# Optimization experiments

Hardware: AMD Instinct MI355X
Metric: run time of the kernel (lower is better)

The kernel has to match this reference:

```python
import jax, jax.numpy as jnp
import numpy as np

B, NQ, T = 1, 16, 512
L, D, H, HD, FF = 8, 512, 8, 64, 2048
LAT, CB, CBD = 1024, 2048, 256


def _rms(x, w, eps=1e-6):
    xf = x.astype(jnp.float32)
    y = xf * jax.lax.rsqrt(jnp.mean(xf * xf, axis=-1, keepdims=True) + eps)
    return y.astype(x.dtype) * w


def _rot_half(x):
    x1, x2 = jnp.split(x, 2, axis=-1)
    return jnp.concatenate((-x2, x1), axis=-1)


def _conv(x, w, b, pad):
    # x: [B, W, Cin], w: [K, Cin, Cout]
    return jax.lax.conv_general_dilated(x, w, (1,), pad, dimension_numbers=('NWC', 'WIO', 'NWC')) + b


def _convT(x, w, b, s):
    # output length = input length * s (SAME-padded transposed conv)
    return jax.lax.conv_transpose(x, w, (s,), 'SAME', dimension_numbers=('NWC', 'WIO', 'NWC')) + b


def setup_inputs() -> dict:
    key = jax.random.key(0)
    ks = iter(jax.random.split(key, 64))
    p = lambda *s: 0.02 * jax.random.normal(next(ks), s, jnp.float32)
    return dict(
        codes=jax.random.randint(next(ks), (B, NQ, T), 0, CB),
        emb_first=p(CB, CBD), pf_w=p(CBD, LAT), pf_b=p(LAT),
        fo_w=p(LAT, LAT), fo_b=p(LAT),
        emb_rest=p(NQ - 1, CB, CBD), pr_w=p(NQ - 1, CBD, LAT), pr_b=p(NQ - 1, LAT),
        ro_w=p(LAT, LAT), ro_b=p(LAT),
        pre_w=p(3, LAT, LAT), pre_b=p(LAT),
        in_w=p(LAT, D), in_b=p(D),
        ln1=jnp.ones((L, D)), qw=p(L, D, D), kw=p(L, D, D), vw=p(L, D, D), ow=p(L, D, D),
        qn=jnp.ones((L, HD)), kn=jnp.ones((L, HD)),
        ls_a=jnp.full((L, D), 0.1), ln2=jnp.ones((L, D)),
        w1=p(L, D, FF), w2=p(L, FF, D), ls_m=jnp.full((L, D), 0.1),
        fn_w=jnp.ones((D,)), out_w=p(D, LAT), out_b=p(LAT),
        up_w=p(4, LAT, LAT), up_b=p(LAT),
        dec0_w=p(7, LAT, 512), dec0_b=p(512),
        dw1=p(16, 512, 256), db1=p(256),
        dw2=p(12, 256, 128), db2=p(128),
        dw3=p(10, 128, 64), db3=p(64),
        dw4=p(8, 64, 32), db4=p(32),
        fin_w=p(7, 32, 1), fin_b=p(1),
    )


def reference(codes, emb_first, pf_w, pf_b, fo_w, fo_b, emb_rest, pr_w, pr_b, ro_w, ro_b,
              pre_w, pre_b, in_w, in_b, ln1, qw, kw, vw, ow, qn, kn, ls_a, ln2, w1, w2,
              ls_m, fn_w, out_w, out_b, up_w, up_b, dec0_w, dec0_b,
              dw1, db1, dw2, db2, dw3, db3, dw4, db4, fin_w, fin_b):
    Bc, _, Tc = codes.shape
    # --- RVQ decode (unrolled codebook lookups + 1x1 output projections) ---
    qf = jnp.take(emb_first, codes[:, 0], axis=0)            # [B,T,CBD]
    qf = qf @ pf_w + pf_b                                    # project_out -> [B,T,LAT]
    qf = qf @ fo_w + fo_b                                    # first_output_proj
    codes_rest = jnp.swapaxes(codes[:, 1:], 0, 1)            # [NQ-1,B,T]
    g = jax.vmap(lambda e, c: jnp.take(e, c, axis=0))(emb_rest, codes_rest)  # [NQ-1,B,T,CBD]
    qr = jnp.einsum('nbtc,ncd->btd', g, pr_w) + jnp.sum(pr_b, axis=0)
    qr = qr @ ro_w + ro_b                                    # rest_output_proj
    hidden = qf + qr                                         # [B,T,LAT]
    # --- causal pre_conv (k=3, left pad) ---
    hidden = _conv(hidden, pre_w, pre_b, [(2, 0)])
    # --- pre_transformer: RoPE + qk-norm + layerscale, manual causal attention ---
    h = hidden @ in_w + in_b                                 # [B,T,D]
    pos = jnp.arange(Tc, dtype=jnp.float32)
    inv_freq = 1.0 / (10000.0 ** (jnp.arange(0, HD, 2, dtype=jnp.float32) / HD))
    freqs = pos[:, None] * inv_freq[None, :]                 # [T,HD/2]
    emb = jnp.concatenate((freqs, freqs), axis=-1)           # [T,HD]
    cos, sin = jnp.cos(emb), jnp.sin(emb)
    mask = jnp.triu(jnp.full((Tc, Tc), -jnp.inf, dtype=jnp.float32), k=1)
    scale = HD ** -0.5
    for l in range(L):
        x = _rms(h, ln1[l])
        q = _rms((x @ qw[l]).reshape(Bc, Tc, H, HD), qn[l]).transpose(0, 2, 1, 3)
        k = _rms((x @ kw[l]).reshape(Bc, Tc, H, HD), kn[l]).transpose(0, 2, 1, 3)
        v = (x @ vw[l]).reshape(Bc, Tc, H, HD).transpose(0, 2, 1, 3)
        q = q * cos + _rot_half(q) * sin
        k = k * cos + _rot_half(k) * sin
        scores = jnp.einsum('bhqd,bhkd->bhqk', q, k) * scale + mask
        a = jax.nn.softmax(scores.astype(jnp.float32), axis=-1).astype(x.dtype)
        o = jnp.einsum('bhqk,bhkd->bhqd', a, v).transpose(0, 2, 1, 3).reshape(Bc, Tc, D)
        h = h + ls_a[l] * (o @ ow[l])
        x = _rms(h, ln2[l])
        h = h + ls_m[l] * (jax.nn.gelu(x @ w1[l], approximate=False) @ w2[l])
    h = _rms(h, fn_w) @ out_w + out_b                        # [B,T,LAT]
    # --- upsample x2 ---
    x = jax.nn.elu(_convT(h, up_w, up_b, 2))
    x = _conv(x, dec0_w, dec0_b, 'SAME')
    for w, b, r in ((dw1, db1, 8), (dw2, db2, 6), (dw3, db3, 5), (dw4, db4, 4)):
        x = _convT(jax.nn.elu(x), w, b, r)
    x = _conv(jax.nn.elu(x), fin_w, fin_b, 'SAME')           # [B,S,1]
    return jnp.clip(jnp.swapaxes(x, 1, 2), -1.0, 1.0)        # [B,1,S]
```

## Files before the change

### kernel.cpp

```cpp
#include <hip/hip_runtime.h>
#include <hip/hip_bf16.h>
#include <math.h>

#define T_LEN 512
#define LAT   1024
#define D_DIM 512
#define NH    8
#define HD    64
#define FF_D  2048
#define NL    8
#define NQ    16

typedef _Float16 f16x4 __attribute__((ext_vector_type(4)));
typedef _Float16 f16x8 __attribute__((ext_vector_type(8)));
typedef float    f32x4 __attribute__((ext_vector_type(4)));

#define WS_QFPRE    0
#define WS_G        131072
#define WS_QF       2097152
#define WS_TA       2621440
#define WS_HIDG     3145728
#define WS_HID      3147776
#define WS_CONV     3672064
#define WS_H        4196352
#define WS_X        4458496
#define WS_QB       4720640
#define WS_KB       4982784
#define WS_VB       5244928
#define WS_ATT      5507072
#define WS_FF       5769216
#define WS_BSUM     6817792
#define WS_HOUT     6819840
#define WS_UP       7348224
#define WS_DEC0     8400384
#define WS_T1       8925440
#define WS_T2       11022976
#define WS_W2UP     17314560
#define WS_W2D1     23606016
#define WS_W2D2     26751744
#define WS_W2D3     27341568
#define WS_T3       31457344
#define WS_W2D4     47186048
#define WS_T4       0
#define WS_DEC0B16  11022976
#define WS_PART     31457344
#define WS_BTPR     35651712
#define WS_ROPE     39583872

__global__ void k_zero_guards(float* __restrict__ ws) {
    const int offs[13] = {3145728, 6818816, 7344128, 7345152, 8396800,
                          8399872, 8924672, 8925184, 11022592, 11022848,
                          17314432, 31457280, 47185984};
    const int lens[13] = {2048, 1024, 1024, 3072, 3072,
                          512, 512, 256, 256, 128,
                          128, 64, 64};
    int r = blockIdx.x;
    for (int i = threadIdx.x; i < lens[r]; i += 256) ws[offs[r] + i] = 0.f;
}

__global__ __launch_bounds__(256) void k_gather(const int* __restrict__ codes,
                                                const float* __restrict__ emb_first,
                                                const float* __restrict__ emb_rest,
                                                float* __restrict__ qf_pre,
                                                float* __restrict__ G) {
    int idx = blockIdx.x * 256 + threadIdx.x;
    int c = idx & 255;
    int r = (idx >> 8) & 15;
    int t = idx >> 12;
    if (t >= T_LEN) return;
    if (r == 0) {
        int code = codes[t];
        qf_pre[t * 256 + c] = emb_first[code * 256 + c];
    } else {
        int n = r - 1;
        int code = codes[(n + 1) * T_LEN + t];
        G[t * 3840 + n * 256 + c] = emb_rest[(n * 2048 + code) * 256 + c];
    }
}

__global__ void k_bias_sum(const float* __restrict__ pr_b, float* __restrict__ out) {
    int d = blockIdx.x * 256 + threadIdx.x;
    if (d >= LAT) return;
    float s = 0.f;
    for (int n = 0; n < NQ - 1; n++) s += pr_b[n * LAT + d];
    out[d] = s;
}

__global__ void k_rope_tab(float* __restrict__ tab) {
    int idx = blockIdx.x * 256 + threadIdx.x;
    int t = idx >> 5, dm = idx & 31;
    double inv = pow(10000.0, -(double)dm / 32.0);
    double ang = (double)t * inv;
    tab[idx] = (float)cos(ang);
    tab[16384 + idx] = (float)sin(ang);
}

__global__ __launch_bounds__(256) void k_wt16(const float* __restrict__ w,
                                              _Float16* __restrict__ bth,
                                              _Float16* __restrict__ btl,
                                              int Cin, int Cout, int s, int pad_a) {
    int K3 = 3 * Cin;
    int col = blockIdx.x * 64 + (threadIdx.x & 63);
    int rk0 = blockIdx.y * 128 + (threadIdx.x >> 6) * 32;
    if (rk0 >= K3) return;
    int p = col / Cout, co = col - p * Cout;
    int kk0 = (pad_a - p) % s;
    if (kk0 < 0) kk0 += s;
    int cp = (p + kk0 - pad_a) / s;
    size_t ob = (size_t)col * K3 + rk0;
    for (int rb = 0; rb < 32; rb += 4) {
        f16x4 h, l;
#pragma unroll
        for (int j2 = 0; j2 < 4; ++j2) {
            int rowk = rk0 + rb + j2;
            int j = rowk / Cin, ci = rowk - j * Cin;
            int d = j - 1;
            float v = 0.f;
            if (d == cp) v = w[((size_t)kk0 * Cin + ci) * Cout + co];
            else if (d == cp + 1) v = w[((size_t)(kk0 + s) * Cin + ci) * Cout + co];
            _Float16 hh = (_Float16)v;
            h[j2] = hh;
            l[j2] = (_Float16)(v - (float)hh);
        }
        *(f16x4*)(bth + ob + rb) = h;
        *(f16x4*)(btl + ob + rb) = l;
    }
}

__global__ __launch_bounds__(256) void k_bt16(const float* __restrict__ w,
                                              _Float16* __restrict__ bth,
                                              _Float16* __restrict__ btl,
                                              int K, int N) {
    int col = blockIdx.x * 64 + (threadIdx.x & 63);
    int rk0 = blockIdx.y * 128 + (threadIdx.x >> 6) * 32;
    size_t ob = (size_t)col * K + rk0;
    for (int rb = 0; rb < 32; rb += 4) {
        f16x4 h, l;
#pragma unroll
        for (int j2 = 0; j2 < 4; ++j2) {
            float v = w[(size_t)(rk0 + rb + j2) * N + col];
            _Float16 hh = (_Float16)v;
            h[j2] = hh;
            l[j2] = (_Float16)(v - (float)hh);
        }
        *(f16x4*)(bth + ob + rb) = h;
        *(f16x4*)(btl + ob + rb) = l;
    }
}

__device__ __forceinline__ float apply_act(float v, int act) {
    if (act == 1) return 0.5f * v * (1.0f + erff(v * 0.70710678118654752440f));
    if (act == 2) return v > 0.f ? v : expm1f(v);
    return v;
}

__global__ __launch_bounds__(256) void k_gemm16(const float* __restrict__ A, int lda,
                                                const _Float16* __restrict__ BTh,
                                                const _Float16* __restrict__ BTl, int ldb,
                                                const float* __restrict__ bias, unsigned bmask,
                                                float* __restrict__ C,
                                                float* __restrict__ part, long mn,
                                                int N, int klen, int act) {
    __shared__ _Float16 Ash[128 * 64];
    __shared__ _Float16 Asl[128 * 64];
    __shared__ _Float16 Bsh[64 * 64];
    __shared__ _Float16 Bsl[64 * 64];
    int tid = threadIdx.x;
    int m0 = blockIdx.x * 128, n0 = blockIdx.y * 64;
    int kz = blockIdx.z * klen;
    const float* Ab = A + kz;
    int lane = tid & 63, wv = tid >> 6;
    int wr = wv >> 1, wc = wv & 1;
    int fr = lane & 15, g = lane >> 4;

    f32x4 acc[4][2];
#pragma unroll
    for (int m = 0; m < 4; ++m)
#pragma unroll
        for (int n = 0; n < 2; ++n)
#pragma unroll
            for (int r = 0; r < 4; ++r) acc[m][n][r] = 0.f;

    int nk = klen >> 6;
    for (int t = 0; t < nk; ++t) {
        int k0 = t << 6;
#pragma unroll
        for (int i2 = 0; i2 < 8; ++i2) {
            int c = tid + 256 * i2;
            int row = c >> 4, kc = c & 15;
            float4 v = *(const float4*)(Ab + (size_t)(m0 + row) * lda + k0 + (kc << 2));
            f16x4 h, l;
            float vv[4] = {v.x, v.y, v.z, v.w};
#pragma unroll
            for (int j = 0; j < 4; ++j) {
                _Float16 hh = (_Float16)vv[j];
                h[j] = hh;
                l[j] = (_Float16)(vv[j] - (float)hh);
            }
            int off = row * 64 + (((kc >> 1) ^ (row & 7)) << 3) + ((kc & 1) << 2);
            *(f16x4*)(Ash + off) = h;
            *(f16x4*)(Asl + off) = l;
        }
#pragma unroll
        for (int i2 = 0; i2 < 2; ++i2) {
            int c = tid + 256 * i2;
            int col = c >> 3, s = c & 7;
            size_t goff = (size_t)(n0 + col) * ldb + kz + k0 + (s << 3);
            f16x8 hv = *(const f16x8*)(BTh + goff);
            f16x8 lv = *(const f16x8*)(BTl + goff);
            int off = col * 64 + ((s ^ (col & 7)) << 3);
            *(f16x8*)(Bsh + off) = hv;
            *(f16x8*)(Bsl + off) = lv;
        }
        __syncthreads();
#pragma unroll
        for (int kk = 0; kk < 2; ++kk) {
            f16x8 ah[4], al[4], bh[2], bl[2];
#pragma unroll
            for (int m = 0; m < 4; ++m) {
                int row = wr * 64 + m * 16 + fr;
                int off = row * 64 + ((((kk << 2) + g) ^ (row & 7)) << 3);
                ah[m] = *(const f16x8*)(Ash + off);
                al[m] = *(const f16x8*)(Asl + off);
            }
#pragma unroll
            for (int n = 0; n < 2; ++n) {
                int col = wc * 32 + n * 16 + fr;
                int off = col * 64 + ((((kk << 2) + g) ^ (col & 7)) << 3);
                bh[n] = *(const f16x8*)(Bsh + off);
                bl[n] = *(const f16x8*)(Bsl + off);
            }
#pragma unroll
            for (int m = 0; m < 4; ++m)
#pragma unroll
                for (int n = 0; n < 2; ++n) {
                    acc[m][n] = __builtin_amdgcn_mfma_f32_16x16x32_f16(ah[m], bh[n], acc[m][n], 0, 0, 0);
                    acc[m][n] = __builtin_amdgcn_mfma_f32_16x16x32_f16(ah[m], bl[n], acc[m][n], 0, 0, 0);
                    acc[m][n] = __builtin_amdgcn_mfma_f32_16x16x32_f16(al[m], bh[n], acc[m][n], 0, 0, 0);
                }
        }
        __syncthreads();
    }
    if (part) {
        float* op = part + (size_t)blockIdx.z * mn;
#pragma unroll
        for (int m = 0; m < 4; ++m) {
            int row = m0 + wr * 64 + m * 16 + (g << 2);
#pragma unroll
            for (int n = 0; n < 2; ++n) {
                int col = n0 + wc * 32 + n * 16 + fr;
#pragma unroll
                for (int r = 0; r < 4; ++r)
                    op[(size_t)(row + r) * N + col] = acc[m][n][r];
            }
        }
    } else {
#pragma unroll
        for (int m = 0; m < 4; ++m) {
            int row = m0 + wr * 64 + m * 16 + (g << 2);
#pragma unroll
            for (int n = 0; n < 2; ++n) {
                int col = n0 + wc * 32 + n * 16 + fr;
                float bv = bias ? bias[col & bmask] : 0.f;
#pragma unroll
                for (int r = 0; r < 4; ++r) {
                    float v = acc[m][n][r] + bv;
                    v = apply_act(v, act);
                    C[(size_t)(row + r) * N + col] = v;
                }
            }
        }
    }
}

template <int TM>
__device__ __forceinline__ void gemm_core(const float* __restrict__ A, int lda,
                                          const float* __restrict__ B, int N,
                                          int klen, int m0, int n0,
                                          float (&acc)[TM / 16][4]) {
    constexpr int RM = TM / 16;
    constexpr int AR = TM * 16 / 256;
    __shared__ float As[2][16][TM + 4];
    __shared__ float Bs[2][16][64];
    int tid = threadIdx.x;
    int tx = tid & 15, ty = tid >> 4;
    int bc = tid & 63, br0 = tid >> 6;
    int arow[AR], akk[AR];
#pragma unroll
    for (int i = 0; i < AR; i++) { int idx = tid + 256 * i; arow[i] = idx >> 4; akk[i] = idx & 15; }
    float areg[AR], breg[4];
#pragma unroll
    for (int i = 0; i < AR; i++) areg[i] = A[(size_t)(m0 + arow[i]) * lda + akk[i]];
#pragma unroll
    for (int i = 0; i < 4; i++) breg[i] = B[(size_t)(br0 + 4 * i) * N + n0 + bc];
#pragma unroll
    for (int i = 0; i < AR; i++) As[0][akk[i]][arow[i]] = areg[i];
#pragma unroll
    for (int i = 0; i < 4; i++) Bs[0][br0 + 4 * i][bc] = breg[i];
    __syncthreads();
    int nk = klen >> 4;
    for (int t = 0; t < nk; t++) {
        int cur = t & 1;
        if (t + 1 < nk) {
            int k0 = (t + 1) << 4;
#pragma unroll
            for (int i = 0; i < AR; i++) areg[i] = A[(size_t)(m0 + arow[i]) * lda + k0 + akk[i]];
#pragma unroll
            for (int i = 0; i < 4; i++) breg[i] = B[(size_t)(k0 + br0 + 4 * i) * N + n0 + bc];
        }
#pragma unroll
        for (int kk = 0; kk < 16; kk++) {
            float a[RM], b[4];
#pragma unroll
            for (int i = 0; i < RM; i++) a[i] = As[cur][kk][ty * RM + i];
#pragma unroll
            for (int j = 0; j < 4; j++) b[j] = Bs[cur][kk][tx * 4 + j];
#pragma unroll
            for (int i = 0; i < RM; i++)
#pragma unroll
                for (int j = 0; j < 4; j++) acc[i][j] += a[i] * b[j];
        }
        if (t + 1 < nk) {
            int nxt = cur ^ 1;
#pragma unroll
            for (int i = 0; i < AR; i++) As[nxt][akk[i]][arow[i]] = areg[i];
#pragma unroll
            for (int i = 0; i < 4; i++) Bs[nxt][br0 + 4 * i][bc] = breg[i];
            __syncthreads();
        }
    }
}

template <int TM>
__global__ __launch_bounds__(256) void k_gemm2(const float* __restrict__ A, int lda,
                                               const float* __restrict__ B,
                                               const float* __restrict__ bias, unsigned bmask,
                                               const float* __restrict__ res,
                                               const float* __restrict__ scale,
                                               float* __restrict__ C,
                                               float* __restrict__ part, long mn,
                                               int N, int klen, int act) {
    constexpr int RM = TM / 16;
    float acc[RM][4] = {};
    int m0 = blockIdx.x * TM, n0 = blockIdx.y * 64;
    int kz = blockIdx.z * klen;
    gemm_core<TM>(A + kz, lda, B + (size_t)kz * N, N, klen, m0, n0, acc);
    int tid = threadIdx.x;
    int tx = tid & 15, ty = tid >> 4;
    if (part) {
        float* out = part + (size_t)blockIdx.z * mn;
#pragma unroll
        for (int i = 0; i < RM; i++)
#pragma unroll
            for (int j = 0; j < 4; j++)
                out[(size_t)(m0 + ty * RM + i) * N + n0 + tx * 4 + j] = acc[i][j];
    } else {
#pragma unroll
        for (int i = 0; i < RM; i++) {
            int row = m0 + ty * RM + i;
#pragma unroll
            for (int j = 0; j < 4; j++) {
                int col = n0 + tx * 4 + j;
                float v = acc[i][j];
                if (bias) v += bias[col & bmask];
                v = apply_act(v, act);
                if (scale) v *= scale[col];
                if (res) v += res[(size_t)row * N + col];
                C[(size_t)row * N + col] = v;
            }
        }
    }
}

__global__ __launch_bounds__(256) void k_qkv(const float* __restrict__ A,
                                             const float* __restrict__ B0,
                                             const float* __restrict__ B1,
                                             const float* __restrict__ B2,
                                             float* __restrict__ part) {
    int which = blockIdx.z >> 1, s = blockIdx.z & 1;
    const float* B = which == 0 ? B0 : (which == 1 ? B1 : B2);
    float acc[2][4] = {};
    int m0 = blockIdx.x * 32, n0 = blockIdx.y * 64;
    int kz = s * 256;
    gemm_core<32>(A + kz, 512, B + (size_t)kz * 512, 512, 256, m0, n0, acc);
    int tid = threadIdx.x;
    int tx = tid & 15, ty = tid >> 4;
    float* out = part + (size_t)blockIdx.z * (512 * 512);
#pragma unroll
    for (int i = 0; i < 2; i++)
#pragma unroll
        for (int j = 0; j < 4; j++)
            out[(size_t)(m0 + ty * 2 + i) * 512 + n0 + tx * 4 + j] = acc[i][j];
}

__global__ __launch_bounds__(256) void k_reduce(const float* __restrict__ part, long mn, int S,
                                                const float* __restrict__ bias, unsigned bmask,
                                                const float* __restrict__ res,
                                                const float* __restrict__ scale,
                                                float* __restrict__ C, int N, int act) {
    long idx = ((long)blockIdx.x * 256 + threadIdx.x) * 4;
    if (idx >= mn) return;
    float4 v = *(const float4*)(part + idx);
    for (int s2 = 1; s2 < S; s2++) {
        float4 u = *(const float4*)(part + (size_t)s2 * mn + idx);
        v.x += u.x; v.y += u.y; v.z += u.z; v.w += u.w;
    }
    int col = (int)(idx % N);
    float vv[4] = {v.x, v.y, v.z, v.w};
#pragma unroll
    for (int j = 0; j < 4; j++) {
        float t = vv[j];
        int c = col + j;
        if (bias) t += bias[c & bmask];
        t = apply_act(t, act);
        if (scale) t *= scale[c];
        if (res) t += res[idx + j];
        vv[j] = t;
    }
    *(float4*)(C + idx) = make_float4(vv[0], vv[1], vv[2], vv[3]);
}

__global__ __launch_bounds__(256) void k_reduce_qkv(const float* __restrict__ part,
                                                    float* __restrict__ q,
                                                    float* __restrict__ k,
                                                    float* __restrict__ v) {
    const long mn = 262144;
    int w = blockIdx.y;
    long idx = ((long)blockIdx.x * 256 + threadIdx.x) * 4;
    float4 a = *(const float4*)(part + (size_t)(2 * w) * mn + idx);
    float4 b = *(const float4*)(part + (size_t)(2 * w + 1) * mn + idx);
    float* C = w == 0 ? q : (w == 1 ? k : v);
    *(float4*)(C + idx) = make_float4(a.x + b.x, a.y + b.y, a.z + b.z, a.w + b.w);
}

__global__ __launch_bounds__(256) void k_rms(const float* __restrict__ x,
                                             const float* __restrict__ g,
                                             float* __restrict__ y, int N) {
    int row = blockIdx.x;
    const float* xr = x + (size_t)row * N;
    int tid = threadIdx.x;
    float s = 0.f;
    for (int i = tid; i < N; i += 256) { float v = xr[i]; s += v * v; }
#pragma unroll
    for (int off = 32; off; off >>= 1) s += __shfl_xor(s, off);
    __shared__ float red[4];
    if ((tid & 63) == 0) red[tid >> 6] = s;
    __syncthreads();
    s = red[0] + red[1] + red[2] + red[3];
    float r = 1.0f / sqrtf(s / (float)N + 1e-6f);
    for (int i = tid; i < N; i += 256) y[(size_t)row * N + i] = xr[i] * r * g[i];
}

__global__ void k_qkrope2(float* __restrict__ q, float* __restrict__ k,
                          const float* __restrict__ gq, const float* __restrict__ gk,
                          const float* __restrict__ tab) {
    int bid = blockIdx.x;
    int t = bid >> 3, h = bid & 7;
    int d = threadIdx.x;
    float* p = (blockIdx.y == 0 ? q : k) + (size_t)t * D_DIM + h * HD;
    const float* g = blockIdx.y == 0 ? gq : gk;
    float val = p[d];
    float s = val * val;
#pragma unroll
    for (int off = 32; off; off >>= 1) s += __shfl_xor(s, off);
    float r = 1.0f / sqrtf(s * (1.0f / 64.0f) + 1e-6f);
    float y = val * r * g[d];
    int dm = d & 31;
    float c = tab[t * 32 + dm];
    float sn = tab[16384 + t * 32 + dm];
    float partner = __shfl_xor(y, 32);
    float out = (d < 32) ? (y * c - partner * sn) : (y * c + partner * sn);
    p[d] = out;
}

__global__ __launch_bounds__(128) void k_attn_mf(const float* __restrict__ q,
                                                 const float* __restrict__ k,
                                                 const float* __restrict__ v,
                                                 float* __restrict__ o) {
    __shared__ _Float16 Ph[2][16][32];
    __shared__ _Float16 Pl[2][16][32];
    __shared__ float mM[16], lM[16], OM[16][64];
    int h = blockIdx.x >> 5, qt = blockIdx.x & 31;
    int qr0 = qt << 4;
    int tid = threadIdx.x;
    int s = tid >> 6, lane = tid & 63;
    int fr = lane & 15, g = lane >> 4;
    int hoff = h * 64;

    f16x8 qh[2], ql[2];
    {
        const float* qp = q + (size_t)(qr0 + fr) * 512 + hoff + g * 8;
#pragma unroll
        for (int c = 0; c < 2; ++c) {
            float4 v0 = *(const float4*)(qp + c * 32);
            float4 v1 = *(const float4*)(qp + c * 32 + 4);
            float vv[8] = {v0.x, v0.y, v0.z, v0.w, v1.x, v1.y, v1.z, v1.w};
#pragma unroll
            for (int j = 0; j < 8; ++j) {
                float x = vv[j] * 0.125f;
                _Float16 hh = (_Float16)x;
                qh[c][j] = hh;
                ql[c][j] = (_Float16)(x - (float)hh);
            }
        }
    }

    float m_run = -3.4e38f, l_run = 0.f;
    f32x4 accO[4];
#pragma unroll
    for (int dt = 0; dt < 4; ++dt)
#pragma unroll
        for (int r = 0; r < 4; ++r) accO[dt][r] = 0.f;

    int nkt = (qr0 + 47) >> 5;
    for (int kt = s; kt < nkt; kt += 2) {
        int c0 = kt << 5;
        float sv[2][4];
        float mx = -3.4e38f;
#pragma unroll
        for (int t2 = 0; t2 < 2; ++t2) {
            const float* kp = k + (size_t)(c0 + t2 * 16 + fr) * 512 + hoff + g * 8;
            f16x8 kh[2], kl[2];
#pragma unroll
            for (int c = 0; c < 2; ++c) {
                float4 v0 = *(const float4*)(kp + c * 32);
                float4 v1 = *(const float4*)(kp + c * 32 + 4);
                float vv[8] = {v0.x, v0.y, v0.z, v0.w, v1.x, v1.y, v1.z, v1.w};
#pragma unroll
                for (int j = 0; j < 8; ++j) {
                    _Float16 hh = (_Float16)vv[j];
                    kh[c][j] = hh;
                    kl[c][j] = (_Float16)(vv[j] - (float)hh);
                }
            }
            f32x4 a;
#pragma unroll
            for (int r = 0; r < 4; ++r) a[r] = 0.f;
#pragma unroll
            for (int c = 0; c < 2; ++c) {
                a = __builtin_amdgcn_mfma_f32_16x16x32_f16(kh[c], qh[c], a, 0, 0, 0);
                a = __builtin_amdgcn_mfma_f32_16x16x32_f16(kh[c], ql[c], a, 0, 0, 0);
                a = __builtin_amdgcn_mfma_f32_16x16x32_f16(kl[c], qh[c], a, 0, 0, 0);
            }
#pragma unroll
            for (int r = 0; r < 4; ++r) {
                int key = c0 + t2 * 16 + g * 4 + r;
                float x = (key <= qr0 + fr) ? a[r] : -3.4e38f;
                sv[t2][r] = x;
                mx = fmaxf(mx, x);
            }
        }
        mx = fmaxf(mx, __shfl_xor(mx, 16));
        mx = fmaxf(mx, __shfl_xor(mx, 32));
        float m_new = fmaxf(m_run, mx);
        float alpha = __expf(m_run - m_new);
        l_run *= alpha;
        float ar[4];
#pragma unroll
        for (int r = 0; r < 4; ++r) ar[r] = __shfl(alpha, g * 4 + r);
#pragma unroll
        for (int dt = 0; dt < 4; ++dt)
#pragma unroll
            for (int r = 0; r < 4; ++r) accO[dt][r] *= ar[r];
        float psum = 0.f;
#pragma unroll
        for (int t2 = 0; t2 < 2; ++t2) {
            f16x4 ph4, pl4;
#pragma unroll
            for (int r = 0; r < 4; ++r) {
                float p = __expf(sv[t2][r] - m_new);
                psum += p;
                _Float16 hh = (_Float16)p;
                ph4[r] = hh;
                pl4[r] = (_Float16)(p - (float)hh);
            }
            *(f16x4*)(&Ph[s][fr][t2 * 16 + g * 4]) = ph4;
            *(f16x4*)(&Pl[s][fr][t2 * 16 + g * 4]) = pl4;
        }
        psum += __shfl_xor(psum, 16);
        psum += __shfl_xor(psum, 32);
        l_run += psum;
        m_run = m_new;
        f16x8 pah = *(const f16x8*)(&Ph[s][fr][g * 8]);
        f16x8 pal = *(const f16x8*)(&Pl[s][fr][g * 8]);
#pragma unroll
        for (int dt = 0; dt < 4; ++dt) {
            const float* vp = v + (size_t)(c0 + g * 8) * 512 + hoff + dt * 16 + fr;
            f16x8 bh, bl;
#pragma unroll
            for (int j = 0; j < 8; ++j) {
                float x = vp[(size_t)j * 512];
                _Float16 hh = (_Float16)x;
                bh[j] = hh;
                bl[j] = (_Float16)(x - (float)hh);
            }
            accO[dt] = __builtin_amdgcn_mfma_f32_16x16x32_f16(pah, bh, accO[dt], 0, 0, 0);
            accO[dt] = __builtin_amdgcn_mfma_f32_16x16x32_f16(pah, bl, accO[dt], 0, 0, 0);
            accO[dt] = __builtin_amdgcn_mfma_f32_16x16x32_f16(pal, bh, accO[dt], 0, 0, 0);
        }
    }
    if (s == 1) {
        if (g == 0) { mM[fr] = m_run; lM[fr] = l_run; }
#pragma unroll
        for (int dt = 0; dt < 4; ++dt)
#pragma unroll
            for (int r = 0; r < 4; ++r)
                OM[g * 4 + r][dt * 16 + fr] = accO[dt][r];
    }
    __syncthreads();
    if (s == 0) {
        float m1 = mM[fr], l1 = lM[fr];
        float mf = fmaxf(m_run, m1);
        float a0 = __expf(m_run - mf), a1 = __expf(m1 - mf);
        float lf = l_run * a0 + l1 * a1;
        float inv = 1.0f / lf;
        float a0r[4], a1r[4], invr[4];
#pragma unroll
        for (int r = 0; r < 4; ++r) {
            a0r[r] = __shfl(a0, g * 4 + r);
            a1r[r] = __shfl(a1, g * 4 + r);
            invr[r] = __shfl(inv, g * 4 + r);
        }
#pragma unroll
        for (int dt = 0; dt < 4; ++dt)
#pragma unroll
            for (int r = 0; r < 4; ++r) {
                float ov = (accO[dt][r] * a0r[r] + OM[g * 4 + r][dt * 16 + fr] * a1r[r]) * invr[r];
                o[(size_t)(qr0 + g * 4 + r) * 512 + hoff + dt * 16 + fr] = ov;
            }
    }
}

__global__ __launch_bounds__(256) void k_conv_fin(const float* __restrict__ x,
                                                  const float* __restrict__ w,
                                                  const float* __restrict__ b,
                                                  float* __restrict__ y, int n) {
    __shared__ float xs[262 * 33];
    __shared__ float wsm[224];
    int tid = threadIdx.x;
    int o0 = blockIdx.x * 256;
    for (int i = tid; i < 262 * 32; i += 256) {
        int r = i >> 5, c = i & 31;
        int t = o0 - 3 + r;
        xs[r * 33 + c] = (t >= 0 && t < n) ? x[(size_t)t * 32 + c] : 0.f;
    }
    if (tid < 224) wsm[tid] = w[tid];
    __syncthreads();
    float acc = b[0];
#pragma unroll
    for (int kk = 0; kk < 7; kk++)
#pragma unroll
        for (int ci = 0; ci < 32; ci++)
            acc += xs[(tid + kk) * 33 + ci] * wsm[kk * 32 + ci];
    y[o0 + tid] = fminf(fmaxf(acc, -1.f), 1.f);
}

static inline void gemmS64(hipStream_t st, const float* A, int lda, const float* B,
                           const float* bias, unsigned bmask, const float* res,
                           const float* scale, float* C, float* part,
                           int M, int N, int K, int S, int act) {
    long mn = (long)M * N;
    if (S > 1) {
        k_gemm2<64><<<dim3(M / 64, N / 64, S), 256, 0, st>>>(
            A, lda, B, nullptr, 0, nullptr, nullptr, nullptr, part, mn, N, K / S, 0);
        k_reduce<<<dim3((int)(mn / 1024)), 256, 0, st>>>(
            part, mn, S, bias, bmask, res, scale, C, N, act);
    } else {
        k_gemm2<64><<<dim3(M / 64, N / 64, 1), 256, 0, st>>>(
            A, lda, B, bias, bmask, res, scale, C, nullptr, mn, N, K, act);
    }
}
static inline void gemmS32(hipStream_t st, const float* A, int lda, const float* B,
                           const float* bias, unsigned bmask, const float* res,
                           const float* scale, float* C, float* part,
                           int M, int N, int K, int S, int act) {
    long mn = (long)M * N;
    if (S > 1) {
        k_gemm2<32><<<dim3(M / 32, N / 64, S), 256, 0, st>>>(
            A, lda, B, nullptr, 0, nullptr, nullptr, nullptr, part, mn, N, K / S, 0);
        k_reduce<<<dim3((int)(mn / 1024)), 256, 0, st>>>(
            part, mn, S, bias, bmask, res, scale, C, N, act);
    } else {
        k_gemm2<32><<<dim3(M / 32, N / 64, 1), 256, 0, st>>>(
            A, lda, B, bias, bmask, res, scale, C, nullptr, mn, N, K, act);
    }
}

extern "C" void kernel_launch(void* const* d_in, const int* in_sizes, int n_in,
                              void* d_out, int out_size, void* d_ws, size_t ws_size,
                              hipStream_t stream) {
    int i = 0;
    const int*   codes     = (const int*)  d_in[i++];
    const float* emb_first = (const float*)d_in[i++];
    const float* pf_w      = (const float*)d_in[i++];
    const float* pf_b      = (const float*)d_in[i++];
    const float* fo_w      = (const float*)d_in[i++];
    const float* fo_b      = (const float*)d_in[i++];
    const float* emb_rest  = (const float*)d_in[i++];
    const float* pr_w      = (const float*)d_in[i++];
    const float* pr_b      = (const float*)d_in[i++];
    const float* ro_w      = (const float*)d_in[i++];
    const float* ro_b      = (const float*)d_in[i++];
    const float* pre_w     = (const float*)d_in[i++];
    const float* pre_b     = (const float*)d_in[i++];
    const float* in_w      = (const float*)d_in[i++];
    const float* in_b      = (const float*)d_in[i++];
    const float* ln1       = (const float*)d_in[i++];
    const float* qw        = (const float*)d_in[i++];
    const float* kw        = (const float*)d_in[i++];
    const float* vw        = (const float*)d_in[i++];
    const float* ow        = (const float*)d_in[i++];
    const float* qn        = (const float*)d_in[i++];
    const float* kn        = (const float*)d_in[i++];
    const float* ls_a      = (const float*)d_in[i++];
    const float* ln2       = (const float*)d_in[i++];
    const float* w1        = (const float*)d_in[i++];
    const float* w2        = (const float*)d_in[i++];
    const float* ls_m      = (const float*)d_in[i++];
    const float* fn_w      = (const float*)d_in[i++];
    const float* out_w     = (const float*)d_in[i++];
    const float* out_b     = (const float*)d_in[i++];
    const float* up_w      = (const float*)d_in[i++];
    const float* up_b      = (const float*)d_in[i++];
    const float* dec0_w    = (const float*)d_in[i++];
    const float* dec0_b    = (const float*)d_in[i++];
    const float* dw1       = (const float*)d_in[i++];
    const float* db1       = (const float*)d_in[i++];
    const float* dw2       = (const float*)d_in[i++];
    const float* db2       = (const float*)d_in[i++];
    const float* dw3       = (const float*)d_in[i++];
    const float* db3       = (const float*)d_in[i++];
    const float* dw4       = (const float*)d_in[i++];
    const float* db4       = (const float*)d_in[i++];
    const float* fin_w     = (const float*)d_in[i++];
    const float* fin_b     = (const float*)d_in[i++];

    float* ws = (float*)d_ws;
    float* outp = (float*)d_out;

    float* qf_pre   = ws + WS_QFPRE;
    float* G        = ws + WS_G;
    float* qf       = ws + WS_QF;
    float* tA       = ws + WS_TA;
    float* hidden   = ws + WS_HID;
    float* conv_out = ws + WS_CONV;
    float* h        = ws + WS_H;
    float* x        = ws + WS_X;
    float* qb       = ws + WS_QB;
    float* kb       = ws + WS_KB;
    float* vb       = ws + WS_VB;
    float* attnb    = ws + WS_ATT;
    float* ff       = ws + WS_FF;
    float* bias_sum = ws + WS_BSUM;
    float* houtp    = ws + WS_HOUT;
    float* up_out   = ws + WS_UP;
    float* dec0_out = ws + WS_DEC0;
    float* t1       = ws + WS_T1;
    float* t2       = ws + WS_T2;
    float* t3       = ws + WS_T3;
    float* t4       = ws + WS_T4;
    float* part     = ws + WS_PART;
    float* ropetab  = ws + WS_ROPE;

    _Float16* BTup_h = (_Float16*)(ws + WS_W2UP);   _Float16* BTup_l = BTup_h + 2048 * 3072;
    _Float16* BTd1_h = (_Float16*)(ws + WS_W2D1);   _Float16* BTd1_l = BTd1_h + 2048 * 1536;
    _Float16* BTd2_h = (_Float16*)(ws + WS_W2D2);   _Float16* BTd2_l = BTd2_h + 768 * 768;
    _Float16* BTd3_h = (_Float16*)(ws + WS_W2D3);   _Float16* BTd3_l = BTd3_h + 320 * 384;
    _Float16* BTd4_h = (_Float16*)(ws + WS_W2D4);   _Float16* BTd4_l = BTd4_h + 128 * 192;
    _Float16* BTd0_h = (_Float16*)(ws + WS_DEC0B16);_Float16* BTd0_l = BTd0_h + 512 * 7168;
    _Float16* BTpr_h = (_Float16*)(ws + WS_BTPR);   _Float16* BTpr_l = BTpr_h + 1024 * 3840;

    k_zero_guards<<<13, 256, 0, stream>>>(ws);
    k_rope_tab<<<64, 256, 0, stream>>>(ropetab);
    k_wt16<<<dim3(32, 24), 256, 0, stream>>>(up_w, BTup_h, BTup_l, 1024, 1024, 2, 2);
    k_wt16<<<dim3(32, 12), 256, 0, stream>>>(dw1, BTd1_h, BTd1_l, 512, 256, 8, 11);
    k_wt16<<<dim3(12, 6), 256, 0, stream>>>(dw2, BTd2_h, BTd2_l, 256, 128, 6, 8);
    k_wt16<<<dim3(5, 3), 256, 0, stream>>>(dw3, BTd3_h, BTd3_l, 128, 64, 5, 7);
    k_wt16<<<dim3(2, 2), 256, 0, stream>>>(dw4, BTd4_h, BTd4_l, 64, 32, 4, 5);
    k_bt16<<<dim3(8, 56), 256, 0, stream>>>(dec0_w, BTd0_h, BTd0_l, 7168, 512);
    k_bt16<<<dim3(16, 30), 256, 0, stream>>>(pr_w, BTpr_h, BTpr_l, 3840, 1024);

    k_gather<<<8192, 256, 0, stream>>>(codes, emb_first, emb_rest, qf_pre, G);
    k_bias_sum<<<4, 256, 0, stream>>>(pr_b, bias_sum);
    gemmS64(stream, qf_pre, 256, pf_w, pf_b, ~0u, nullptr, nullptr, tA, part, 512, 1024, 256, 2, 0);
    gemmS64(stream, tA, 1024, fo_w, fo_b, ~0u, nullptr, nullptr, qf, part, 512, 1024, 1024, 4, 0);
    k_gemm16<<<dim3(4, 16, 4), 256, 0, stream>>>(G, 3840, BTpr_h, BTpr_l, 3840,
            nullptr, 0, nullptr, part, 524288L, 1024, 960, 0);
    k_reduce<<<512, 256, 0, stream>>>(part, 524288L, 4, bias_sum, ~0u, nullptr, nullptr,
            tA, 1024, 0);
    gemmS64(stream, tA, 1024, ro_w, ro_b, ~0u, qf, nullptr, hidden, part, 512, 1024, 1024, 4, 0);

    gemmS64(stream, hidden - 2048, 1024, pre_w, pre_b, ~0u, nullptr, nullptr,
            conv_out, part, 512, 1024, 3072, 8, 0);

    gemmS32(stream, conv_out, 1024, in_w, in_b, ~0u, nullptr, nullptr, h, part, 512, 512, 1024, 4, 0);

    for (int l = 0; l < NL; l++) {
        const float* qw_l = qw + (size_t)l * D_DIM * D_DIM;
        const float* kw_l = kw + (size_t)l * D_DIM * D_DIM;
        const float* vw_l = vw + (size_t)l * D_DIM * D_DIM;
        const float* ow_l = ow + (size_t)l * D_DIM * D_DIM;
        const float* w1_l = w1 + (size_t)l * D_DIM * FF_D;
        const float* w2_l = w2 + (size_t)l * FF_D * D_DIM;

        k_rms<<<512, 256, 0, stream>>>(h, ln1 + l * D_DIM, x, D_DIM);
        k_qkv<<<dim3(16, 8, 6), 256, 0, stream>>>(x, qw_l, kw_l, vw_l, part);
        k_reduce_qkv<<<dim3(256, 3), 256, 0, stream>>>(part, qb, kb, vb);
        k_qkrope2<<<dim3(T_LEN * NH, 2), 64, 0, stream>>>(qb, kb, qn + l * HD, kn + l * HD, ropetab);
        k_attn_mf<<<256, 128, 0, stream>>>(qb, kb, vb, attnb);
        gemmS32(stream, attnb, 512, ow_l, nullptr, 0, h, ls_a + l * D_DIM, h, part,
                512, 512, 512, 2, 0);
        k_rms<<<512, 256, 0, stream>>>(h, ln2 + l * D_DIM, x, D_DIM);
        gemmS64(stream, x, 512, w1_l, nullptr, 0, nullptr, nullptr, ff, part,
                512, 2048, 512, 2, 1);
        gemmS32(stream, ff, 2048, w2_l, nullptr, 0, h, ls_m + l * D_DIM, h, part,
                512, 512, 2048, 8, 0);
    }

    k_rms<<<512, 256, 0, stream>>>(h, fn_w, x, D_DIM);
    gemmS64(stream, x, 512, out_w, out_b, ~0u, nullptr, nullptr, houtp, part, 512, 1024, 512, 4, 0);

    k_gemm16<<<dim3(4, 32, 2), 256, 0, stream>>>(houtp - 1024, 1024, BTup_h, BTup_l, 3072,
            nullptr, 0, nullptr, part, 1048576L, 2048, 1536, 0);
    k_reduce<<<1024, 256, 0, stream>>>(part, 1048576L, 2, up_b, 1023u, nullptr, nullptr,
            up_out, 2048, 2);

    k_gemm16<<<dim3(8, 8, 4), 256, 0, stream>>>(up_out - 3072, 1024, BTd0_h, BTd0_l, 7168,
            nullptr, 0, nullptr, part, 524288L, 512, 1792, 0);
    k_reduce<<<512, 256, 0, stream>>>(part, 524288L, 4, dec0_b, ~0u, nullptr, nullptr,
            dec0_out, 512, 2);

    k_gemm16<<<dim3(8, 32, 1), 256, 0, stream>>>(dec0_out - 512, 512, BTd1_h, BTd1_l, 1536,
            db1, 255u, t1, nullptr, 0L, 2048, 1536, 2);
    k_gemm16<<<dim3(64, 12, 1), 256, 0, stream>>>(t1 - 256, 256, BTd2_h, BTd2_l, 768,
            db2, 127u, t2, nullptr, 0L, 768, 768, 2);
    k_gemm16<<<dim3(384, 5, 1), 256, 0, stream>>>(t2 - 128, 128, BTd3_h, BTd3_l, 384,
            db3, 63u, t3, nullptr, 0L, 320, 384, 2);
    k_gemm16<<<dim3(1920, 2, 1), 256, 0, stream>>>(t3 - 64, 64, BTd4_h, BTd4_l, 192,
            db4, 31u, t4, nullptr, 0L, 128, 192, 2);

    k_conv_fin<<<983040 / 256, 256, 0, stream>>>(t4, fin_w, fin_b, outp, 983040);
}
```

Baseline: 2.033 ms.

## Store decoder activations as pre-split fp16 hi/lo pairs feeding new MFMA GEMM

The decoder chain now writes its intermediate activations directly as fp16 high/low split pairs, either from the GEMM epilogue or from a new reduce kernel. A new templated GEMM, k_gemm16h, loads these pre-split A operands with vector loads into swizzled shared memory. This removes the per-tile fp32-to-fp16 split of A inside each GEMM and halves activation traffic per component. Tile widths and split-K counts are also retuned per layer. The cost is a more complicated workspace layout with extra guard-zeroing regions, which could produce aliasing bugs.

```diff
diff --git a/kernel.cpp b/kernel.cpp
--- a/kernel.cpp
+++ b/kernel.cpp
@@ -31,15 +31,20 @@
 #define WS_FF       5769216
 #define WS_BSUM     6817792
 #define WS_HOUT     6819840
-#define WS_UP       7348224
-#define WS_DEC0     8400384
-#define WS_T1       8925440
-#define WS_T2       11022976
+#define UP16H_D   7346688
+#define UP16L_D   7874048
+#define DEC16H_D  8400128
+#define DEC16L_D  8662784
+#define T1H_D     8925312
+#define T1L_D     9974144
+#define T2H_D     11022912
+#define T2L_D     14168768
+#define T3H_D     31457312
+#define T3L_D     39321696
 #define WS_W2UP     17314560
 #define WS_W2D1     23606016
 #define WS_W2D2     26751744
 #define WS_W2D3     27341568
-#define WS_T3       31457344
 #define WS_W2D4     47186048
 #define WS_T4       0
 #define WS_DEC0B16  11022976
@@ -48,12 +53,22 @@
 #define WS_ROPE     39583872
 
 __global__ void k_zero_guards(float* __restrict__ ws) {
-    const int offs[13] = {3145728, 6818816, 7344128, 7345152, 8396800,
-                          8399872, 8924672, 8925184, 11022592, 11022848,
-                          17314432, 31457280, 47185984};
-    const int lens[13] = {2048, 1024, 1024, 3072, 3072,
-                          512, 512, 256, 256, 128,
-                          128, 64, 64};
+    const int offs[15] = {3145728, 6818816, 7344128,
+                          7345152, 7870976, 7872512, 8398336,
+                          8399872, 8662272, 8662528, 8924928,
+                          8925184, 9973888, 9974016, 11022720};
+    const int lens[15] = {2048, 1024, 1024,
+                          1536, 1536, 1536, 1536,
+                          256, 256, 256, 256,
+                          128, 128, 128, 128};
+    int r = blockIdx.x;
+    for (int i = threadIdx.x; i < lens[r]; i += 256) ws[offs[r] + i] = 0.f;
+}
+
+__global__ void k_zero2(float* __restrict__ ws) {
+    const int offs[8] = {11022848, 14168640, 14168704, 17314496,
+                         31457280, 39321632, 39321664, 47186016};
+    const int lens[8] = {64, 64, 64, 64, 32, 32, 32, 32};
     int r = blockIdx.x;
     for (int i = threadIdx.x; i < lens[r]; i += 256) ws[offs[r] + i] = 0.f;
 }
@@ -273,6 +288,126 @@
     }
 }
 
+template <int NT>
+__global__ __launch_bounds__(256) void k_gemm16h(
+        const _Float16* __restrict__ Ah, const _Float16* __restrict__ Al, int lda,
+        const _Float16* __restrict__ BTh, const _Float16* __restrict__ BTl, int ldb,
+        const float* __restrict__ bias, unsigned bmask,
+        float* __restrict__ C, _Float16* __restrict__ Ch, _Float16* __restrict__ Cl,
+        float* __restrict__ part, long mn, int N, int klen, int act) {
+    constexpr int BN = NT * 32;
+    __shared__ _Float16 Ash[128 * 64];
+    __shared__ _Float16 Asl[128 * 64];
+    __shared__ _Float16 Bsh[BN * 64];
+    __shared__ _Float16 Bsl[BN * 64];
+    int tid = threadIdx.x;
+    int m0 = blockIdx.x * 128, n0 = blockIdx.y * BN;
+    int kz = blockIdx.z * klen;
+    int lane = tid & 63, wv = tid >> 6;
+    int wr = wv >> 1, wc = wv & 1;
+    int fr = lane & 15, g = lane >> 4;
+
+    f32x4 acc[4][NT];
+#pragma unroll
+    for (int m = 0; m < 4; ++m)
+#pragma unroll
+        for (int n = 0; n < NT; ++n)
+#pragma unroll
+            for (int r = 0; r < 4; ++r) acc[m][n][r] = 0.f;
+
+    int nk = klen >> 6;
+    for (int t = 0; t < nk; ++t) {
+        int k0 = kz + (t << 6);
+#pragma unroll
+        for (int i2 = 0; i2 < 4; ++i2) {
+            int c = tid + 256 * i2;
+            int row = c >> 3, s = c & 7;
+            size_t go = (size_t)(m0 + row) * lda + k0 + (s << 3);
+            f16x8 hv = *(const f16x8*)(Ah + go);
+            f16x8 lv = *(const f16x8*)(Al + go);
+            int off = row * 64 + ((s ^ (row & 7)) << 3);
+            *(f16x8*)(Ash + off) = hv;
+            *(f16x8*)(Asl + off) = lv;
+        }
+#pragma unroll
+        for (int i2 = 0; i2 < BN / 32; ++i2) {
+            int c = tid + 256 * i2;
+            int col = c >> 3, s = c & 7;
+            size_t go = (size_t)(n0 + col) * ldb + k0 + (s << 3);
+            f16x8 hv = *(const f16x8*)(BTh + go);
+            f16x8 lv = *(const f16x8*)(BTl + go);
+            int off = col * 64 + ((s ^ (col & 7)) << 3);
+            *(f16x8*)(Bsh + off) = hv;
+            *(f16x8*)(Bsl + off) = lv;
+        }
+        __syncthreads();
+#pragma unroll
+        for (int kk = 0; kk < 2; ++kk) {
+            f16x8 ah[4], al4[4], bh[NT], bl[NT];
+#pragma unroll
+            for (int m = 0; m < 4; ++m) {
+                int row = wr * 64 + m * 16 + fr;
+                int off = row * 64 + ((((kk << 2) + g) ^ (row & 7)) << 3);
+                ah[m] = *(const f16x8*)(Ash + off);
+                al4[m] = *(const f16x8*)(Asl + off);
+            }
+#pragma unroll
+            for (int n = 0; n < NT; ++n) {
+                int col = wc * (NT * 16) + n * 16 + fr;
+                int off = col * 64 + ((((kk << 2) + g) ^ (col & 7)) << 3);
+                bh[n] = *(const f16x8*)(Bsh + off);
+                bl[n] = *(const f16x8*)(Bsl + off);
+            }
+#pragma unroll
+            for (int m = 0; m < 4; ++m)
+#pragma unroll
+                for (int n = 0; n < NT; ++n) {
+                    acc[m][n] = __builtin_amdgcn_mfma_f32_16x16x32_f16(ah[m], bh[n], acc[m][n], 0, 0, 0);
+                    acc[m][n] = __builtin_amdgcn_mfma_f32_16x16x32_f16(ah[m], bl[n], acc[m][n], 0, 0, 0);
+                    acc[m][n] = __builtin_amdgcn_mfma_f32_16x16x32_f16(al4[m], bh[n], acc[m][n], 0, 0, 0);
+                }
+        }
+        __syncthreads();
+    }
+    if (part) {
+        float* op = part + (size_t)blockIdx.z * mn;
+#pragma unroll
+        for (int m = 0; m < 4; ++m) {
+            int row = m0 + wr * 64 + m * 16 + (g << 2);
+#pragma unroll
+            for (int n = 0; n < NT; ++n) {
+                int col = n0 + wc * (NT * 16) + n * 16 + fr;
+#pragma unroll
+                for (int r = 0; r < 4; ++r)
+                    op[(size_t)(row + r) * N + col] = acc[m][n][r];
+            }
+        }
+    } else {
+#pragma unroll
+        for (int m = 0; m < 4; ++m) {
+            int row = m0 + wr * 64 + m * 16 + (g << 2);
+#pragma unroll
+            for (int n = 0; n < NT; ++n) {
+                int col = n0 + wc * (NT * 16) + n * 16 + fr;
+                float bv = bias ? bias[col & bmask] : 0.f;
+#pragma unroll
+                for (int r = 0; r < 4; ++r) {
+                    float v = acc[m][n][r] + bv;
+                    v = apply_act(v, act);
+                    size_t idx = (size_t)(row + r) * N + col;
+                    if (Cl) {
+                        _Float16 hh = (_Float16)v;
+                        Ch[idx] = hh;
+                        Cl[idx] = (_Float16)(v - (float)hh);
+                    } else {
+                        C[idx] = v;
+                    }
+                }
+            }
+        }
+    }
+}
+
 template <int TM>
 __device__ __forceinline__ void gemm_core(const float* __restrict__ A, int lda,
                                           const float* __restrict__ B, int N,
@@ -418,6 +553,33 @@
         vv[j] = t;
     }
     *(float4*)(C + idx) = make_float4(vv[0], vv[1], vv[2], vv[3]);
+}
+
+__global__ __launch_bounds__(256) void k_reduce_h(const float* __restrict__ part, long mn, int S,
+                                                  const float* __restrict__ bias, unsigned bmask,
+                                                  _Float16* __restrict__ Ch,
+                                                  _Float16* __restrict__ Cl, int N, int act) {
+    long idx = ((long)blockIdx.x * 256 + threadIdx.x) * 4;
+    if (idx >= mn) return;
+    float4 v = *(const float4*)(part + idx);
+    for (int s2 = 1; s2 < S; s2++) {
+        float4 u = *(const float4*)(part + (size_t)s2 * mn + idx);
+        v.x += u.x; v.y += u.y; v.z += u.z; v.w += u.w;
+    }
+    int col = (int)(idx % N);
+    float vv[4] = {v.x, v.y, v.z, v.w};
+    f16x4 h, l;
+#pragma unroll
+    for (int j = 0; j < 4; j++) {
+        float t = vv[j];
+        if (bias) t += bias[(col + j) & bmask];
+        t = apply_act(t, act);
+        _Float16 hh = (_Float16)t;
+        h[j] = hh;
+        l[j] = (_Float16)(t - (float)hh);
+    }
+    *(f16x4*)(Ch + idx) = h;
+    *(f16x4*)(Cl + idx) = l;
 }
 
 __global__ __launch_bounds__(256) void k_reduce_qkv(const float* __restrict__ part,
@@ -753,14 +915,20 @@
     float* ff       = ws + WS_FF;
     float* bias_sum = ws + WS_BSUM;
     float* houtp    = ws + WS_HOUT;
-    float* up_out   = ws + WS_UP;
-    float* dec0_out = ws + WS_DEC0;
-    float* t1       = ws + WS_T1;
-    float* t2       = ws + WS_T2;
-    float* t3       = ws + WS_T3;
     float* t4       = ws + WS_T4;
     float* part     = ws + WS_PART;
     float* ropetab  = ws + WS_ROPE;
+
+    _Float16* up16h = (_Float16*)(ws + UP16H_D);
+    _Float16* up16l = (_Float16*)(ws + UP16L_D);
+    _Float16* dec16h = (_Float16*)(ws + DEC16H_D);
+    _Float16* dec16l = (_Float16*)(ws + DEC16L_D);
+    _Float16* t1h = (_Float16*)(ws + T1H_D);
+    _Float16* t1l = (_Float16*)(ws + T1L_D);
+    _Float16* t2h = (_Float16*)(ws + T2H_D);
+    _Float16* t2l = (_Float16*)(ws + T2L_D);
+    _Float16* t3h = (_Float16*)(ws + T3H_D);
+    _Float16* t3l = (_Float16*)(ws + T3L_D);
 
     _Float16* BTup_h = (_Float16*)(ws + WS_W2UP);   _Float16* BTup_l = BTup_h + 2048 * 3072;
     _Float16* BTd1_h = (_Float16*)(ws + WS_W2D1);   _Float16* BTd1_l = BTd1_h + 2048 * 1536;
@@ -770,7 +938,7 @@
     _Float16* BTd0_h = (_Float16*)(ws + WS_DEC0B16);_Float16* BTd0_l = BTd0_h + 512 * 7168;
     _Float16* BTpr_h = (_Float16*)(ws + WS_BTPR);   _Float16* BTpr_l = BTpr_h + 1024 * 3840;
 
-    k_zero_guards<<<13, 256, 0, stream>>>(ws);
+    k_zero_guards<<<15, 256, 0, stream>>>(ws);
     k_rope_tab<<<64, 256, 0, stream>>>(ropetab);
     k_wt16<<<dim3(32, 24), 256, 0, stream>>>(up_w, BTup_h, BTup_l, 1024, 1024, 2, 2);
     k_wt16<<<dim3(32, 12), 256, 0, stream>>>(dw1, BTd1_h, BTd1_l, 512, 256, 8, 11);
@@ -822,22 +990,24 @@
 
     k_gemm16<<<dim3(4, 32, 2), 256, 0, stream>>>(houtp - 1024, 1024, BTup_h, BTup_l, 3072,
             nullptr, 0, nullptr, part, 1048576L, 2048, 1536, 0);
-    k_reduce<<<1024, 256, 0, stream>>>(part, 1048576L, 2, up_b, 1023u, nullptr, nullptr,
-            up_out, 2048, 2);
-
-    k_gemm16<<<dim3(8, 8, 4), 256, 0, stream>>>(up_out - 3072, 1024, BTd0_h, BTd0_l, 7168,
-            nullptr, 0, nullptr, part, 524288L, 512, 1792, 0);
-    k_reduce<<<512, 256, 0, stream>>>(part, 524288L, 4, dec0_b, ~0u, nullptr, nullptr,
-            dec0_out, 512, 2);
-
-    k_gemm16<<<dim3(8, 32, 1), 256, 0, stream>>>(dec0_out - 512, 512, BTd1_h, BTd1_l, 1536,
-            db1, 255u, t1, nullptr, 0L, 2048, 1536, 2);
-    k_gemm16<<<dim3(64, 12, 1), 256, 0, stream>>>(t1 - 256, 256, BTd2_h, BTd2_l, 768,
-            db2, 127u, t2, nullptr, 0L, 768, 768, 2);
-    k_gemm16<<<dim3(384, 5, 1), 256, 0, stream>>>(t2 - 128, 128, BTd3_h, BTd3_l, 384,
-            db3, 63u, t3, nullptr, 0L, 320, 384, 2);
-    k_gemm16<<<dim3(1920, 2, 1), 256, 0, stream>>>(t3 - 64, 64, BTd4_h, BTd4_l, 192,
-            db4, 31u, t4, nullptr, 0L, 128, 192, 2);
+    k_reduce_h<<<1024, 256, 0, stream>>>(part, 1048576L, 2, up_b, 1023u,
+            up16h, up16l, 2048, 2);
+
+    k_gemm16h<4><<<dim3(8, 4, 8), 256, 0, stream>>>(up16h - 3072, up16l - 3072, 1024,
+            BTd0_h, BTd0_l, 7168, nullptr, 0, nullptr, nullptr, nullptr,
+            part, 524288L, 512, 896, 0);
+    k_reduce_h<<<512, 256, 0, stream>>>(part, 524288L, 8, dec0_b, ~0u,
+            dec16h, dec16l, 512, 2);
+    k_zero2<<<8, 256, 0, stream>>>(ws);
+
+    k_gemm16h<2><<<dim3(8, 32, 1), 256, 0, stream>>>(dec16h - 512, dec16l - 512, 512,
+            BTd1_h, BTd1_l, 1536, db1, 255u, nullptr, t1h, t1l, nullptr, 0L, 2048, 1536, 2);
+    k_gemm16h<4><<<dim3(64, 6, 1), 256, 0, stream>>>(t1h - 256, t1l - 256, 256,
+            BTd2_h, BTd2_l, 768, db2, 127u, nullptr, t2h, t2l, nullptr, 0L, 768, 768, 2);
+    k_gemm16h<2><<<dim3(384, 5, 1), 256, 0, stream>>>(t2h - 128, t2l - 128, 128,
+            BTd3_h, BTd3_l, 384, db3, 63u, nullptr, t3h, t3l, nullptr, 0L, 320, 384, 2);
+    k_gemm16h<4><<<dim3(1920, 1, 1), 256, 0, stream>>>(t3h - 64, t3l - 64, 64,
+            BTd4_h, BTd4_l, 192, db4, 31u, t4, nullptr, nullptr, nullptr, 0L, 128, 192, 2);
 
     k_conv_fin<<<983040 / 256, 256, 0, stream>>>(t4, fin_w, fin_b, outp, 983040);
 }
```

Measured after the change: 2.006 ms. Within noise of the previous version (-1.3%).
